# Performance work log

Measured on AMD Instinct MI355X. Metric: run time of the kernel, lower is better.

## Reference

```python
import jax, jax.numpy as jnp
import numpy as np

N_EMBD = 1024
HEAD_SIZE = 64
N_HEADS = 16
BLOCK_SIZE = 2048


def setup_inputs() -> dict:
    key = jax.random.key(0)
    ks = jax.random.split(key, 7)
    s = 0.02
    return {
        "X": jax.random.normal(ks[0], (2, BLOCK_SIZE, N_EMBD), dtype=jnp.float32),
        # per-head projection weights, torch Linear layout [out, in] stacked over heads
        "Wq": jax.random.normal(ks[1], (N_HEADS, HEAD_SIZE, N_EMBD), dtype=jnp.float32) * s,
        "Wk": jax.random.normal(ks[2], (N_HEADS, HEAD_SIZE, N_EMBD), dtype=jnp.float32) * s,
        "Wv": jax.random.normal(ks[3], (N_HEADS, HEAD_SIZE, N_EMBD), dtype=jnp.float32) * s,
        "Wp": jax.random.normal(ks[4], (N_EMBD, N_EMBD), dtype=jnp.float32) * s,
        "bp": jax.random.normal(ks[5], (N_EMBD,), dtype=jnp.float32) * s,
    }


def reference(X, Wq, Wk, Wv, Wp, bp):
    B, T, C = X.shape
    # per-head projections: [B,H,T,D]
    q = jnp.einsum("btc,hdc->bhtd", X, Wq)
    k = jnp.einsum("btc,hdc->bhtd", X, Wk)
    v = jnp.einsum("btc,hdc->bhtd", X, Wv)
    # NOTE: original scales by C**-0.5 where C = n_embd (not head_size)
    scores = jnp.einsum("bhtd,bhsd->bhts", q, k) * (C ** -0.5)  # [B,H,T,T]
    causal = jnp.tril(jnp.ones((T, T), dtype=bool))
    scores = jnp.where(causal, scores, -jnp.inf)
    weights = jax.nn.softmax(scores, axis=-1)
    out = jnp.einsum("bhts,bhsd->bhtd", weights, v)  # [B,H,T,D]
    # concat heads along last dim: [B,T,H*D]
    out = out.transpose(0, 2, 1, 3).reshape(B, T, -1)
    # output projection (dropout is identity in eval)
    return out @ Wp.T + bp
```

## Files before the change

### kernel.cpp

```cpp
#include <hip/hip_runtime.h>
#include <hip/hip_bf16.h>

typedef __bf16 bf16_t;
typedef __bf16 bf16x8 __attribute__((ext_vector_type(8)));
typedef __bf16 bf16x4 __attribute__((ext_vector_type(4)));
typedef float  f32x4  __attribute__((ext_vector_type(4)));
typedef unsigned int u32x4 __attribute__((ext_vector_type(4)));

#define MFMA16(a,b,c) __builtin_amdgcn_mfma_f32_16x16x32_bf16(a,b,c,0,0,0)

constexpr int B_ = 2, T_ = 2048, H_ = 16, D_ = 64, C_ = 1024;
constexpr int GK = C_;

typedef const __attribute__((address_space(1))) unsigned char ga_t;
typedef __attribute__((address_space(3))) unsigned char la_t;
__device__ __forceinline__ void gld16(const void* g, void* l) {
  __builtin_amdgcn_global_load_lds((ga_t*)g, (la_t*)l, 16, 0, 0);
}

__global__ __launch_bounds__(256) void cast_all(
    const float* __restrict__ X,  const float* __restrict__ Wq,
    const float* __restrict__ Wk, const float* __restrict__ Wv,
    const float* __restrict__ Wp,
    bf16_t* __restrict__ Xb,  bf16_t* __restrict__ Wqb, bf16_t* __restrict__ Wkb,
    bf16_t* __restrict__ Wvb, bf16_t* __restrict__ Wpb)
{
  int i = blockIdx.x * 256 + threadIdx.x;
  const float* src; bf16_t* dst; int off;
  if      (i < 1048576) { src = X;  dst = Xb;  off = i; }
  else if (i < 1310720) { src = Wq; dst = Wqb; off = i - 1048576; }
  else if (i < 1572864) { src = Wk; dst = Wkb; off = i - 1310720; }
  else if (i < 1835008) { src = Wv; dst = Wvb; off = i - 1572864; }
  else                  { src = Wp; dst = Wpb; off = i - 1835008; }
  float4 v = *reinterpret_cast<const float4*>(src + (size_t)off * 4);
  bf16x4 o;
  o[0] = (bf16_t)v.x; o[1] = (bf16_t)v.y; o[2] = (bf16_t)v.z; o[3] = (bf16_t)v.w;
  *reinterpret_cast<bf16x4*>(dst + (size_t)off * 4) = o;
}

__device__ __forceinline__ void gemm128_core(
    const bf16_t* __restrict__ A, const bf16_t* __restrict__ Bw,
    bf16_t* sA, bf16_t* sB, f32x4 (&acc)[4][2], int bx, int by)
{
  const int tid = threadIdx.x, lane = tid & 63, wid = tid >> 6;
  const int wm = wid >> 2, wn = wid & 3;
  const int g = lane >> 4, c = lane & 15, rk = c & 7;
  const int srow = tid >> 3;
  const int sg   = (tid & 7) ^ (srow & 7);
  const bf16_t* asrc = A  + (size_t)(bx * 128 + srow) * GK + sg * 8;
  const bf16_t* bsrc = Bw + (size_t)(by * 128 + srow) * GK + sg * 8;

  #define STGP(buf, kt)                                                       \
    { char* da = (char*)sA + (buf) * 16384;                                   \
      char* db = (char*)sB + (buf) * 16384;                                   \
      _Pragma("unroll")                                                       \
      for (int it = 0; it < 2; ++it) {                                        \
        gld16(asrc + (size_t)it * 65536 + (kt) * 64, da + (it * 512 + tid) * 16); \
        gld16(bsrc + (size_t)it * 65536 + (kt) * 64, db + (it * 512 + tid) * 16); \
      } }

  #define ITERP(t, buf)                                                       \
    {                                                                         \
      if ((t) < 15) asm volatile("s_waitcnt vmcnt(4)");                       \
      else          asm volatile("s_waitcnt vmcnt(0)");                       \
      __builtin_amdgcn_s_barrier();                                           \
      __builtin_amdgcn_sched_barrier(0);                                      \
      const char* ca = (const char*)sA + (buf) * 16384;                       \
      const char* cb = (const char*)sB + (buf) * 16384;                       \
      bf16x8 af[4][2], bfr[2][2];                                             \
      _Pragma("unroll")                                                       \
      for (int mi = 0; mi < 4; ++mi)                                          \
        _Pragma("unroll")                                                     \
        for (int ks = 0; ks < 2; ++ks)                                        \
          af[mi][ks] = *reinterpret_cast<const bf16x8*>(                      \
              ca + (wm * 64 + mi * 16 + c) * 128 + (((ks * 4 + g) ^ rk) * 16)); \
      _Pragma("unroll")                                                       \
      for (int ni = 0; ni < 2; ++ni)                                          \
        _Pragma("unroll")                                                     \
        for (int ks = 0; ks < 2; ++ks)                                        \
          bfr[ni][ks] = *reinterpret_cast<const bf16x8*>(                     \
              cb + (wn * 32 + ni * 16 + c) * 128 + (((ks * 4 + g) ^ rk) * 16)); \
      asm volatile("s_waitcnt lgkmcnt(0)");                                   \
      __builtin_amdgcn_sched_barrier(0);                                      \
      __builtin_amdgcn_s_barrier();                                           \
      __builtin_amdgcn_sched_barrier(0);                                      \
      if ((t) + 2 < 16) STGP(buf, (t) + 2);                                   \
      __builtin_amdgcn_s_setprio(1);                                          \
      _Pragma("unroll")                                                       \
      for (int ks = 0; ks < 2; ++ks)                                          \
        _Pragma("unroll")                                                     \
        for (int mi = 0; mi < 4; ++mi)                                        \
          _Pragma("unroll")                                                   \
          for (int ni = 0; ni < 2; ++ni)                                      \
            acc[mi][ni] = MFMA16(af[mi][ks], bfr[ni][ks], acc[mi][ni]);       \
      __builtin_amdgcn_s_setprio(0);                                          \
    }

  STGP(0, 0);
  STGP(1, 1);
  #pragma unroll 1
  for (int t0 = 0; t0 < 16; t0 += 2) {
    ITERP(t0, 0);
    ITERP(t0 + 1, 1);
  }
  #undef ITERP
  #undef STGP
}

__global__ __launch_bounds__(512, 2) void gemm_qkv(
    const bf16_t* __restrict__ Xb, const bf16_t* __restrict__ Wqkv,
    bf16_t* __restrict__ qo, bf16_t* __restrict__ ko, bf16_t* __restrict__ vto)
{
  __shared__ bf16_t sA[2][128 * 64];
  __shared__ bf16_t sB[2][128 * 64];
  f32x4 acc[4][2] = {};
  const int bx = blockIdx.x, by = blockIdx.y;
  gemm128_core(Xb, Wqkv, &sA[0][0], &sB[0][0], acc, bx, by);

  const int tid = threadIdx.x, lane = tid & 63, wid = tid >> 6;
  const int wm = wid >> 2, wn = wid & 3;
  const int g = lane >> 4, c = lane & 15;
  const float qscale = 0.04508422002778f;
  const int mode = by >> 3;
  #pragma unroll
  for (int ni = 0; ni < 2; ++ni) {
    int col = by * 128 + wn * 32 + ni * 16 + c;
    int cm  = col & 1023;
    int h = cm >> 6, d = cm & 63;
    #pragma unroll
    for (int mi = 0; mi < 4; ++mi) {
      int row0 = bx * 128 + wm * 64 + mi * 16 + g * 4;
      int b = row0 >> 11, tt0 = row0 & 2047;
      if (mode == 2) {
        bf16x4 wv;
        #pragma unroll
        for (int r = 0; r < 4; ++r) wv[r] = (bf16_t)acc[mi][ni][r];
        *reinterpret_cast<bf16x4*>(
            &vto[((size_t)(b * H_ + h) * D_ + d) * T_ + tt0]) = wv;
      } else {
        bf16_t* dst = (mode == 0) ? qo : ko;
        float   sc  = (mode == 0) ? qscale : 1.0f;
        #pragma unroll
        for (int r = 0; r < 4; ++r)
          dst[((size_t)(b * H_ + h) * T_ + (tt0 + r)) * D_ + d] =
              (bf16_t)(acc[mi][ni][r] * sc);
      }
    }
  }
}

__global__ __launch_bounds__(256, 4) void attn_fwd(
    const bf16_t* __restrict__ q, const bf16_t* __restrict__ k,
    const bf16_t* __restrict__ vt, bf16_t* __restrict__ att)
{
  __shared__ bf16_t sK[2][64 * 64], sV[2][64 * 64];
  const int tid = threadIdx.x, lane = tid & 63, w = tid >> 6;
  const int g = lane >> 4, c = lane & 15;
  const int bid = blockIdx.x;
  const int qt = 31 - (bid >> 5);
  const int bh = bid & 31;
  const bf16_t* qb = q  + (size_t)bh * T_ * D_;
  const bf16_t* kb = k  + (size_t)bh * T_ * D_;
  const bf16_t* vb = vt + (size_t)bh * D_ * T_;

  bf16x8 qa[2];
  #pragma unroll
  for (int ks = 0; ks < 2; ++ks)
    qa[ks] = *reinterpret_cast<const bf16x8*>(
        qb + (size_t)(qt * 64 + w * 16 + c) * D_ + ks * 32 + g * 8);

  const int srow = tid >> 3, sgr0 = tid & 7;
  #define STAGE(buf, kt)                                                        \
    {                                                                           \
      char* kdst = (char*)sK + (size_t)(buf) * 8192;                            \
      char* vdst = (char*)sV + (size_t)(buf) * 8192;                            \
      _Pragma("unroll")                                                         \
      for (int it = 0; it < 2; ++it) {                                          \
        int idx = it * 256 + tid;                                               \
        int row = it * 32 + srow;                                               \
        int sg  = sgr0 ^ (row & 7);                                             \
        gld16(kb + (size_t)((kt) * 64 + row) * D_ + sg * 8, kdst + idx * 16);   \
        gld16(vb + (size_t)row * T_ + (kt) * 64 + sg * 8,   vdst + idx * 16);   \
      }                                                                         \
    }

  STAGE(0, 0);
  if (qt >= 1) STAGE(1, 1);

  float l_r = 0.f;
  f32x4 acc_t[4] = {};
  const int rowK = c & 7;

  #pragma unroll 1
  for (int kt = 0; kt <= qt; ++kt) {
    const int cur = kt & 1;
    if (kt < qt) asm volatile("s_waitcnt vmcnt(4)");
    else         asm volatile("s_waitcnt vmcnt(0)");
    __builtin_amdgcn_s_barrier();
    __builtin_amdgcn_sched_barrier(0);

    const char* kc = (char*)sK + (size_t)cur * 8192;
    const char* vc = (char*)sV + (size_t)cur * 8192;
    bf16x8 kf[2][4], vf[2][4];
    #pragma unroll
    for (int ks = 0; ks < 2; ++ks)
      #pragma unroll
      for (int f = 0; f < 4; ++f) {
        int rb = (f * 16 + c) * 128;
        int gsw = ((ks * 4 + g) ^ rowK) * 16;
        kf[ks][f] = *reinterpret_cast<const bf16x8*>(kc + rb + gsw);
        vf[ks][f] = *reinterpret_cast<const bf16x8*>(vc + rb + gsw);
      }
    asm volatile("s_waitcnt lgkmcnt(0)");
    __builtin_amdgcn_sched_barrier(0);
    __builtin_amdgcn_s_barrier();
    __builtin_amdgcn_sched_barrier(0);
    if (kt + 2 <= qt) STAGE(cur, kt + 2);

    f32x4 s[4];
    #pragma unroll
    for (int fj = 0; fj < 4; ++fj) {
      s[fj][0] = -8.f; s[fj][1] = -8.f; s[fj][2] = -8.f; s[fj][3] = -8.f;
    }
    __builtin_amdgcn_s_setprio(1);
    #pragma unroll
    for (int fj = 0; fj < 4; ++fj)
      #pragma unroll
      for (int ks = 0; ks < 2; ++ks)
        s[fj] = MFMA16(kf[ks][fj], qa[ks], s[fj]);
    __builtin_amdgcn_s_setprio(0);

    if (kt == qt) {
      #pragma unroll
      for (int fj = 0; fj < 4; ++fj)
        #pragma unroll
        for (int r = 0; r < 4; ++r)
          if (fj * 16 + g * 4 + r > w * 16 + c) s[fj][r] = -1e30f;
    }

    unsigned pk[4][2];
    float ls[4];
    #pragma unroll
    for (int fj = 0; fj < 4; ++fj) {
      float pe0 = __builtin_amdgcn_exp2f(s[fj][0]);
      float pe1 = __builtin_amdgcn_exp2f(s[fj][1]);
      float pe2 = __builtin_amdgcn_exp2f(s[fj][2]);
      float pe3 = __builtin_amdgcn_exp2f(s[fj][3]);
      ls[fj] = (pe0 + pe1) + (pe2 + pe3);
      asm("v_cvt_pk_bf16_f32 %0, %1, %2" : "=v"(pk[fj][0]) : "v"(pe0), "v"(pe1));
      asm("v_cvt_pk_bf16_f32 %0, %1, %2" : "=v"(pk[fj][1]) : "v"(pe2), "v"(pe3));
    }
    l_r += (ls[0] + ls[1]) + (ls[2] + ls[3]);

    bf16x8 pf[2];
    #pragma unroll
    for (int ks = 0; ks < 2; ++ks) {
      unsigned x0 = pk[2 * ks][0], y0 = pk[2 * ks + 1][0];
      unsigned x1 = pk[2 * ks][1], y1 = pk[2 * ks + 1][1];
      asm("v_permlane32_swap_b32 %0, %1" : "+v"(x0), "+v"(y0));
      asm("v_permlane32_swap_b32 %0, %1" : "+v"(x1), "+v"(y1));
      asm("v_permlane16_swap_b32 %0, %1" : "+v"(x0), "+v"(y0));
      asm("v_permlane16_swap_b32 %0, %1" : "+v"(x1), "+v"(y1));
      u32x4 t; t[0] = x0; t[1] = x1; t[2] = y0; t[3] = y1;
      pf[ks] = __builtin_bit_cast(bf16x8, t);
    }

    __builtin_amdgcn_s_setprio(1);
    #pragma unroll
    for (int fd = 0; fd < 4; ++fd)
      #pragma unroll
      for (int ks = 0; ks < 2; ++ks)
        acc_t[fd] = MFMA16(vf[ks][fd], pf[ks], acc_t[fd]);
    __builtin_amdgcn_s_setprio(0);
  }

  l_r += __shfl_xor(l_r, 16);
  l_r += __shfl_xor(l_r, 32);
  float inv = 1.0f / l_r;
  const int b = bh >> 4, h = bh & 15;
  const int t = qt * 64 + w * 16 + c;
  #pragma unroll
  for (int fd = 0; fd < 4; ++fd) {
    bf16x4 wv;
    #pragma unroll
    for (int r = 0; r < 4; ++r) wv[r] = (bf16_t)(acc_t[fd][r] * inv);
    int d = fd * 16 + g * 4;
    *reinterpret_cast<bf16x4*>(&att[((size_t)(b * T_ + t) * H_ + h) * D_ + d]) = wv;
  }
  #undef STAGE
}

__global__ __launch_bounds__(512, 2) void gemm_proj(
    const bf16_t* __restrict__ attb, const bf16_t* __restrict__ Wpb,
    const float* __restrict__ bp, float* __restrict__ out)
{
  __shared__ bf16_t sA[2][128 * 64];
  __shared__ bf16_t sB[2][128 * 64];
  f32x4 acc[4][2] = {};
  const int bx = blockIdx.x, by = blockIdx.y;
  gemm128_core(attb, Wpb, &sA[0][0], &sB[0][0], acc, bx, by);

  const int tid = threadIdx.x, lane = tid & 63, wid = tid >> 6;
  const int wm = wid >> 2, wn = wid & 3;
  const int g = lane >> 4, c = lane & 15;
  #pragma unroll
  for (int m = 0; m < 4; ++m)
    #pragma unroll
    for (int n = 0; n < 2; ++n)
      #pragma unroll
      for (int r = 0; r < 4; ++r) {
        int row = bx * 128 + wm * 64 + m * 16 + g * 4 + r;
        int col = by * 128 + wn * 32 + n * 16 + c;
        out[(size_t)row * C_ + col] = acc[m][n][r] + bp[col];
      }
}

extern "C" void kernel_launch(void* const* d_in, const int* in_sizes, int n_in,
                              void* d_out, int out_size, void* d_ws, size_t ws_size,
                              hipStream_t stream)
{
  const float* X  = (const float*)d_in[0];
  const float* Wq = (const float*)d_in[1];
  const float* Wk = (const float*)d_in[2];
  const float* Wv = (const float*)d_in[3];
  const float* Wp = (const float*)d_in[4];
  const float* bp = (const float*)d_in[5];
  float* out = (float*)d_out;

  char* ws = (char*)d_ws;
  bf16_t* Xb   = (bf16_t*)(ws);
  bf16_t* Wqb  = (bf16_t*)(ws + ((size_t)8  << 20));
  bf16_t* Wkb  = (bf16_t*)(ws + ((size_t)10 << 20));
  bf16_t* Wvb  = (bf16_t*)(ws + ((size_t)12 << 20));
  bf16_t* Wpb  = (bf16_t*)(ws + ((size_t)14 << 20));
  bf16_t* qo   = (bf16_t*)(ws + ((size_t)16 << 20));
  bf16_t* ko   = (bf16_t*)(ws + ((size_t)24 << 20));
  bf16_t* vto  = (bf16_t*)(ws + ((size_t)32 << 20));
  bf16_t* attb = (bf16_t*)(ws + ((size_t)40 << 20));

  cast_all<<<8192, 256, 0, stream>>>(X, Wq, Wk, Wv, Wp, Xb, Wqb, Wkb, Wvb, Wpb);
  gemm_qkv<<<dim3(32, 24), 512, 0, stream>>>(Xb, Wqb, qo, ko, vto);
  attn_fwd<<<1024, 256, 0, stream>>>(qo, ko, vto, attb);
  gemm_proj<<<dim3(32, 8), 512, 0, stream>>>(attb, Wpb, bp, out);
}
```

Baseline: 87.65 us.

## Split attention waves 2x2 over query and key halves with LDS reduction

Each wave in the attention kernel now takes 32 query rows and one 32-key half of each 64-key tile, where before it took 16 query rows and all 64 keys. This halves the LDS fragment reads for K and V per wave and reuses each K and V fragment across two query groups. The two key-half partial accumulators and row sums are then combined through LDS after the loop. The cost is more accumulator registers, an extra barrier and reduction at the end, and half the waves sitting idle during the final store.

After: 89.70 us. +2.3%, slower.

```diff
diff --git a/kernel.cpp b/kernel.cpp
--- a/kernel.cpp
+++ b/kernel.cpp
@@ -155,6 +155,7 @@
 {
   __shared__ bf16_t sK[2][64 * 64], sV[2][64 * 64];
   const int tid = threadIdx.x, lane = tid & 63, w = tid >> 6;
+  const int jh = w >> 1, qh = w & 1;
   const int g = lane >> 4, c = lane & 15;
   const int bid = blockIdx.x;
   const int qt = 31 - (bid >> 5);
@@ -163,11 +164,13 @@
   const bf16_t* kb = k  + (size_t)bh * T_ * D_;
   const bf16_t* vb = vt + (size_t)bh * D_ * T_;
 
-  bf16x8 qa[2];
+  bf16x8 qa[2][2];
   #pragma unroll
-  for (int ks = 0; ks < 2; ++ks)
-    qa[ks] = *reinterpret_cast<const bf16x8*>(
-        qb + (size_t)(qt * 64 + w * 16 + c) * D_ + ks * 32 + g * 8);
+  for (int qg = 0; qg < 2; ++qg)
+    #pragma unroll
+    for (int ks = 0; ks < 2; ++ks)
+      qa[qg][ks] = *reinterpret_cast<const bf16x8*>(
+          qb + (size_t)(qt * 64 + qh * 32 + qg * 16 + c) * D_ + ks * 32 + g * 8);
 
   const int srow = tid >> 3, sgr0 = tid & 7;
   #define STAGE(buf, kt)                                                        \
@@ -187,8 +190,8 @@
   STAGE(0, 0);
   if (qt >= 1) STAGE(1, 1);
 
-  float l_r = 0.f;
-  f32x4 acc_t[4] = {};
+  float l_r[2] = {0.f, 0.f};
+  f32x4 acc[4][2] = {};
   const int rowK = c & 7;
 
   #pragma unroll 1
@@ -201,91 +204,131 @@
 
     const char* kc = (char*)sK + (size_t)cur * 8192;
     const char* vc = (char*)sV + (size_t)cur * 8192;
-    bf16x8 kf[2][4], vf[2][4];
+    bf16x8 kf[2][2], vf[4];
     #pragma unroll
     for (int ks = 0; ks < 2; ++ks)
       #pragma unroll
-      for (int f = 0; f < 4; ++f) {
-        int rb = (f * 16 + c) * 128;
-        int gsw = ((ks * 4 + g) ^ rowK) * 16;
-        kf[ks][f] = *reinterpret_cast<const bf16x8*>(kc + rb + gsw);
-        vf[ks][f] = *reinterpret_cast<const bf16x8*>(vc + rb + gsw);
-      }
+      for (int fj = 0; fj < 2; ++fj)
+        kf[ks][fj] = *reinterpret_cast<const bf16x8*>(
+            kc + (jh * 32 + fj * 16 + c) * 128 + (((ks * 4 + g) ^ rowK) * 16));
+    #pragma unroll
+    for (int fd = 0; fd < 4; ++fd)
+      vf[fd] = *reinterpret_cast<const bf16x8*>(
+          vc + (fd * 16 + c) * 128 + (((jh * 4 + g) ^ rowK) * 16));
     asm volatile("s_waitcnt lgkmcnt(0)");
     __builtin_amdgcn_sched_barrier(0);
     __builtin_amdgcn_s_barrier();
     __builtin_amdgcn_sched_barrier(0);
     if (kt + 2 <= qt) STAGE(cur, kt + 2);
 
-    f32x4 s[4];
-    #pragma unroll
-    for (int fj = 0; fj < 4; ++fj) {
-      s[fj][0] = -8.f; s[fj][1] = -8.f; s[fj][2] = -8.f; s[fj][3] = -8.f;
-    }
+    f32x4 s[2][2];
+    #pragma unroll
+    for (int fj = 0; fj < 2; ++fj)
+      #pragma unroll
+      for (int qg = 0; qg < 2; ++qg) {
+        s[fj][qg][0] = -8.f; s[fj][qg][1] = -8.f;
+        s[fj][qg][2] = -8.f; s[fj][qg][3] = -8.f;
+      }
     __builtin_amdgcn_s_setprio(1);
     #pragma unroll
-    for (int fj = 0; fj < 4; ++fj)
-      #pragma unroll
-      for (int ks = 0; ks < 2; ++ks)
-        s[fj] = MFMA16(kf[ks][fj], qa[ks], s[fj]);
+    for (int fj = 0; fj < 2; ++fj)
+      #pragma unroll
+      for (int qg = 0; qg < 2; ++qg)
+        #pragma unroll
+        for (int ks = 0; ks < 2; ++ks)
+          s[fj][qg] = MFMA16(kf[ks][fj], qa[qg][ks], s[fj][qg]);
     __builtin_amdgcn_s_setprio(0);
 
     if (kt == qt) {
       #pragma unroll
-      for (int fj = 0; fj < 4; ++fj)
-        #pragma unroll
-        for (int r = 0; r < 4; ++r)
-          if (fj * 16 + g * 4 + r > w * 16 + c) s[fj][r] = -1e30f;
-    }
-
-    unsigned pk[4][2];
-    float ls[4];
-    #pragma unroll
-    for (int fj = 0; fj < 4; ++fj) {
-      float pe0 = __builtin_amdgcn_exp2f(s[fj][0]);
-      float pe1 = __builtin_amdgcn_exp2f(s[fj][1]);
-      float pe2 = __builtin_amdgcn_exp2f(s[fj][2]);
-      float pe3 = __builtin_amdgcn_exp2f(s[fj][3]);
-      ls[fj] = (pe0 + pe1) + (pe2 + pe3);
-      asm("v_cvt_pk_bf16_f32 %0, %1, %2" : "=v"(pk[fj][0]) : "v"(pe0), "v"(pe1));
-      asm("v_cvt_pk_bf16_f32 %0, %1, %2" : "=v"(pk[fj][1]) : "v"(pe2), "v"(pe3));
-    }
-    l_r += (ls[0] + ls[1]) + (ls[2] + ls[3]);
+      for (int fj = 0; fj < 2; ++fj)
+        #pragma unroll
+        for (int qg = 0; qg < 2; ++qg)
+          #pragma unroll
+          for (int r = 0; r < 4; ++r)
+            if (jh * 32 + fj * 16 + g * 4 + r > qh * 32 + qg * 16 + c)
+              s[fj][qg][r] = -1e30f;
+    }
+
+    unsigned pk[2][2][2];
+    #pragma unroll
+    for (int fj = 0; fj < 2; ++fj)
+      #pragma unroll
+      for (int qg = 0; qg < 2; ++qg) {
+        float pe0 = __builtin_amdgcn_exp2f(s[fj][qg][0]);
+        float pe1 = __builtin_amdgcn_exp2f(s[fj][qg][1]);
+        float pe2 = __builtin_amdgcn_exp2f(s[fj][qg][2]);
+        float pe3 = __builtin_amdgcn_exp2f(s[fj][qg][3]);
+        l_r[qg] += (pe0 + pe1) + (pe2 + pe3);
+        asm("v_cvt_pk_bf16_f32 %0, %1, %2" : "=v"(pk[fj][qg][0]) : "v"(pe0), "v"(pe1));
+        asm("v_cvt_pk_bf16_f32 %0, %1, %2" : "=v"(pk[fj][qg][1]) : "v"(pe2), "v"(pe3));
+      }
 
     bf16x8 pf[2];
     #pragma unroll
-    for (int ks = 0; ks < 2; ++ks) {
-      unsigned x0 = pk[2 * ks][0], y0 = pk[2 * ks + 1][0];
-      unsigned x1 = pk[2 * ks][1], y1 = pk[2 * ks + 1][1];
+    for (int qg = 0; qg < 2; ++qg) {
+      unsigned x0 = pk[0][qg][0], y0 = pk[1][qg][0];
+      unsigned x1 = pk[0][qg][1], y1 = pk[1][qg][1];
       asm("v_permlane32_swap_b32 %0, %1" : "+v"(x0), "+v"(y0));
       asm("v_permlane32_swap_b32 %0, %1" : "+v"(x1), "+v"(y1));
       asm("v_permlane16_swap_b32 %0, %1" : "+v"(x0), "+v"(y0));
       asm("v_permlane16_swap_b32 %0, %1" : "+v"(x1), "+v"(y1));
       u32x4 t; t[0] = x0; t[1] = x1; t[2] = y0; t[3] = y1;
-      pf[ks] = __builtin_bit_cast(bf16x8, t);
+      pf[qg] = __builtin_bit_cast(bf16x8, t);
     }
 
     __builtin_amdgcn_s_setprio(1);
     #pragma unroll
     for (int fd = 0; fd < 4; ++fd)
       #pragma unroll
-      for (int ks = 0; ks < 2; ++ks)
-        acc_t[fd] = MFMA16(vf[ks][fd], pf[ks], acc_t[fd]);
+      for (int qg = 0; qg < 2; ++qg)
+        acc[fd][qg] = MFMA16(vf[fd], pf[qg], acc[fd][qg]);
     __builtin_amdgcn_s_setprio(0);
   }
 
-  l_r += __shfl_xor(l_r, 16);
-  l_r += __shfl_xor(l_r, 32);
-  float inv = 1.0f / l_r;
-  const int b = bh >> 4, h = bh & 15;
-  const int t = qt * 64 + w * 16 + c;
   #pragma unroll
-  for (int fd = 0; fd < 4; ++fd) {
-    bf16x4 wv;
-    #pragma unroll
-    for (int r = 0; r < 4; ++r) wv[r] = (bf16_t)(acc_t[fd][r] * inv);
-    int d = fd * 16 + g * 4;
-    *reinterpret_cast<bf16x4*>(&att[((size_t)(b * T_ + t) * H_ + h) * D_ + d]) = wv;
+  for (int qg = 0; qg < 2; ++qg) {
+    l_r[qg] += __shfl_xor(l_r[qg], 16);
+    l_r[qg] += __shfl_xor(l_r[qg], 32);
+  }
+
+  float* red  = (float*)&sK[0][0];
+  float* lred = (float*)&sV[0][0];
+  if (jh == 1) {
+    float* dst = red + qh * 2048 + lane * 32;
+    #pragma unroll
+    for (int fd = 0; fd < 4; ++fd)
+      #pragma unroll
+      for (int qg = 0; qg < 2; ++qg)
+        *reinterpret_cast<f32x4*>(dst + (fd * 2 + qg) * 4) = acc[fd][qg];
+    lred[qh * 128 + lane * 2]     = l_r[0];
+    lred[qh * 128 + lane * 2 + 1] = l_r[1];
+  }
+  __syncthreads();
+  if (jh == 0) {
+    const float* src = red + qh * 2048 + lane * 32;
+    #pragma unroll
+    for (int fd = 0; fd < 4; ++fd)
+      #pragma unroll
+      for (int qg = 0; qg < 2; ++qg)
+        acc[fd][qg] += *reinterpret_cast<const f32x4*>(src + (fd * 2 + qg) * 4);
+    l_r[0] += lred[qh * 128 + lane * 2];
+    l_r[1] += lred[qh * 128 + lane * 2 + 1];
+
+    const int b = bh >> 4, h = bh & 15;
+    #pragma unroll
+    for (int qg = 0; qg < 2; ++qg) {
+      float inv = 1.0f / l_r[qg];
+      const int t = qt * 64 + qh * 32 + qg * 16 + c;
+      #pragma unroll
+      for (int fd = 0; fd < 4; ++fd) {
+        bf16x4 wv;
+        #pragma unroll
+        for (int r = 0; r < 4; ++r) wv[r] = (bf16_t)(acc[fd][qg][r] * inv);
+        int d = fd * 16 + g * 4;
+        *reinterpret_cast<bf16x4*>(&att[((size_t)(b * T_ + t) * H_ + h) * D_ + d]) = wv;
+      }
+    }
   }
   #undef STAGE
 }
```

## Enlarge QKV GEMM tiles to 256x256 with a custom interleaved LDS/MFMA loop

Applied to the files above, without the earlier changes.

Replaces the shared 128x128 GEMM core in the QKV projection with an inline 256x256-tile kernel. Each of the 8 waves now computes a 128x64 sub-tile (8x4 accumulators), and the grid shrinks from 768 to 192 blocks. The main loop is hand-scheduled: it splits LDS fragment reads into phases interleaved with MFMA groups and issues the next stage's global-to-LDS loads mid-iteration. The aim is more operand reuse per LDS byte and fewer global loads. The cost is lower CU occupancy with only 192 blocks, plus higher register and LDS pressure per block.

New measurement: 93.42 us. 1.07x slower.

```diff
diff --git a/kernel.cpp b/kernel.cpp
--- a/kernel.cpp
+++ b/kernel.cpp
@@ -111,25 +111,101 @@
     const bf16_t* __restrict__ Xb, const bf16_t* __restrict__ Wqkv,
     bf16_t* __restrict__ qo, bf16_t* __restrict__ ko, bf16_t* __restrict__ vto)
 {
-  __shared__ bf16_t sA[2][128 * 64];
-  __shared__ bf16_t sB[2][128 * 64];
-  f32x4 acc[4][2] = {};
-  const int bx = blockIdx.x, by = blockIdx.y;
-  gemm128_core(Xb, Wqkv, &sA[0][0], &sB[0][0], acc, bx, by);
-
+  __shared__ bf16_t sA[2][256 * 64];
+  __shared__ bf16_t sB[2][256 * 64];
   const int tid = threadIdx.x, lane = tid & 63, wid = tid >> 6;
   const int wm = wid >> 2, wn = wid & 3;
-  const int g = lane >> 4, c = lane & 15;
+  const int g = lane >> 4, c = lane & 15, rk = c & 7;
+  const int bx = blockIdx.x, by = blockIdx.y;
+  const int srow = tid >> 3;
+  const int sg   = (tid & 7) ^ (srow & 7);
+  const bf16_t* asrc = Xb   + (size_t)(bx * 256 + srow) * GK + sg * 8;
+  const bf16_t* bsrc = Wqkv + (size_t)(by * 256 + srow) * GK + sg * 8;
+  f32x4 acc[8][4] = {};
+
+  #define STG(buf, kt)                                                        \
+    { char* da = (char*)sA + (buf) * 32768;                                   \
+      char* db = (char*)sB + (buf) * 32768;                                   \
+      _Pragma("unroll")                                                       \
+      for (int it = 0; it < 4; ++it)                                          \
+        gld16(asrc + (size_t)it * 65536 + (kt) * 64, da + (it * 512 + tid) * 16); \
+      _Pragma("unroll")                                                       \
+      for (int it = 0; it < 4; ++it)                                          \
+        gld16(bsrc + (size_t)it * 65536 + (kt) * 64, db + (it * 512 + tid) * 16); \
+    }
+
+  #define RD_A(dst, mi)                                                       \
+    _Pragma("unroll")                                                         \
+    for (int ks = 0; ks < 2; ++ks)                                            \
+      dst[ks] = *reinterpret_cast<const bf16x8*>(                             \
+          ca + (wm * 128 + (mi) * 16 + c) * 128 + (((ks * 4 + g) ^ rk) * 16));
+  #define RD_B(dst, ni)                                                       \
+    _Pragma("unroll")                                                         \
+    for (int ks = 0; ks < 2; ++ks)                                            \
+      dst[ks] = *reinterpret_cast<const bf16x8*>(                             \
+          cb + (wn * 64 + (ni) * 16 + c) * 128 + (((ks * 4 + g) ^ rk) * 16));
+  #define MM16(ah, nlo, accrow)                                               \
+    __builtin_amdgcn_s_setprio(1);                                            \
+    _Pragma("unroll")                                                         \
+    for (int ks = 0; ks < 2; ++ks)                                            \
+      _Pragma("unroll")                                                       \
+      for (int i = 0; i < 4; ++i)                                             \
+        _Pragma("unroll")                                                     \
+        for (int n = 0; n < 2; ++n)                                           \
+          acc[(accrow) + i][(nlo) + n] =                                      \
+              MFMA16(ah[i][ks], bfr[(nlo) + n][ks], acc[(accrow) + i][(nlo) + n]); \
+    __builtin_amdgcn_s_setprio(0);
+
+  STG(0, 0);
+  STG(1, 1);
+  #pragma unroll 1
+  for (int t = 0; t < 16; ++t) {
+    const int cur = t & 1;
+    if (t < 15) asm volatile("s_waitcnt vmcnt(8)");
+    else        asm volatile("s_waitcnt vmcnt(0)");
+    __builtin_amdgcn_s_barrier();
+    __builtin_amdgcn_sched_barrier(0);
+    const char* ca = (const char*)sA + cur * 32768;
+    const char* cb = (const char*)sB + cur * 32768;
+
+    bf16x8 afr[4][2], bfr[4][2];
+    #pragma unroll
+    for (int i = 0; i < 4; ++i) { RD_A(afr[i], i) }
+    #pragma unroll
+    for (int n = 0; n < 2; ++n) { RD_B(bfr[n], n) }
+    asm volatile("s_waitcnt lgkmcnt(0)");
+    __builtin_amdgcn_sched_barrier(0);
+    MM16(afr, 0, 0)
+    #pragma unroll
+    for (int n = 2; n < 4; ++n) { RD_B(bfr[n], n) }
+    asm volatile("s_waitcnt lgkmcnt(0)");
+    __builtin_amdgcn_sched_barrier(0);
+    MM16(afr, 2, 0)
+    #pragma unroll
+    for (int i = 0; i < 4; ++i) { RD_A(afr[i], 4 + i) }
+    asm volatile("s_waitcnt lgkmcnt(0)");
+    __builtin_amdgcn_sched_barrier(0);
+    MM16(afr, 2, 4)
+    __builtin_amdgcn_s_barrier();
+    __builtin_amdgcn_sched_barrier(0);
+    if (t + 2 < 16) STG(cur, t + 2);
+    MM16(afr, 0, 4)
+  }
+  #undef MM16
+  #undef RD_B
+  #undef RD_A
+  #undef STG
+
   const float qscale = 0.04508422002778f;
-  const int mode = by >> 3;
+  const int mode = by >> 2;
   #pragma unroll
-  for (int ni = 0; ni < 2; ++ni) {
-    int col = by * 128 + wn * 32 + ni * 16 + c;
+  for (int ni = 0; ni < 4; ++ni) {
+    int col = by * 256 + wn * 64 + ni * 16 + c;
     int cm  = col & 1023;
     int h = cm >> 6, d = cm & 63;
     #pragma unroll
-    for (int mi = 0; mi < 4; ++mi) {
-      int row0 = bx * 128 + wm * 64 + mi * 16 + g * 4;
+    for (int mi = 0; mi < 8; ++mi) {
+      int row0 = bx * 256 + wm * 128 + mi * 16 + g * 4;
       int b = row0 >> 11, tt0 = row0 & 2047;
       if (mode == 2) {
         bf16x4 wv;
@@ -339,7 +415,7 @@
   bf16_t* attb = (bf16_t*)(ws + ((size_t)40 << 20));
 
   cast_all<<<8192, 256, 0, stream>>>(X, Wq, Wk, Wv, Wp, Xb, Wqb, Wkb, Wvb, Wpb);
-  gemm_qkv<<<dim3(32, 24), 512, 0, stream>>>(Xb, Wqb, qo, ko, vto);
+  gemm_qkv<<<dim3(16, 12), 512, 0, stream>>>(Xb, Wqb, qo, ko, vto);
   attn_fwd<<<1024, 256, 0, stream>>>(qo, ko, vto, attb);
   gemm_proj<<<dim3(32, 8), 512, 0, stream>>>(attb, Wpb, bp, out);
 }
```
